# Kernel optimization log

Measured on AMD Instinct MI355X. Metric: run time of the kernel, lower is better.

## Reference

```python
import jax, jax.numpy as jnp
import numpy as np

L, H, D, FF = 6, 16, 768, 3072
B, N = 4, 1023
HD = D // H  # 48
EPS = 1e-5


def _layernorm(x, w, b):
    m = jnp.mean(x, axis=-1, keepdims=True)
    v = jnp.mean((x - m) ** 2, axis=-1, keepdims=True)
    return (x - m) / jnp.sqrt(v + EPS) * w + b


def setup_inputs() -> dict:
    key = jax.random.key(0)
    ks = jax.random.split(key, 10)
    ratio = 2.0 ** (-8.0 / H)
    slopes = np.array([ratio ** (i + 1) for i in range(H)], dtype=np.float32)
    return {
        "cls_tokens": jax.random.normal(ks[0], (B, N, D), jnp.float32),
        "cls_token": jax.random.normal(ks[1], (1, 1, D), jnp.float32) * 0.02,
        "log_slopes": jnp.log(jnp.asarray(slopes)),
        "Wqkv": jax.random.normal(ks[2], (L, 3 * D, D), jnp.float32) * 0.02,
        "Wo": jax.random.normal(ks[3], (L, D, D), jnp.float32) * 0.02,
        "Wg": jax.random.normal(ks[4], (L, FF, D), jnp.float32) * 0.02,
        "Wu": jax.random.normal(ks[5], (L, FF, D), jnp.float32) * 0.02,
        "Wd": jax.random.normal(ks[6], (L, D, FF), jnp.float32) * 0.02,
        "ln1_w": jnp.ones((L, D), jnp.float32),
        "ln1_b": jnp.zeros((L, D), jnp.float32),
        "ln2_w": jnp.ones((L, D), jnp.float32),
        "ln2_b": jnp.zeros((L, D), jnp.float32),
        "fin_w": jnp.ones((D,), jnp.float32),
        "fin_b": jnp.zeros((D,), jnp.float32),
    }


def reference(cls_tokens, cls_token, log_slopes, Wqkv, Wo, Wg, Wu, Wd,
              ln1_w, ln1_b, ln2_w, ln2_b, fin_w, fin_b):
    b, n, dmodel = cls_tokens.shape
    S = n + 1
    # learnable ALiBi: -exp(log_slope) * |i - j|, shape (H, S, S)
    pos = jnp.arange(S)
    dist = jnp.abs(pos[None, :] - pos[:, None]).astype(cls_tokens.dtype)
    bias = -(jnp.exp(log_slopes)[:, None, None] * dist[None, :, :])

    x = jnp.concatenate([jnp.broadcast_to(cls_token, (b, 1, dmodel)), cls_tokens], axis=1)
    scale = 1.0 / jnp.sqrt(jnp.asarray(HD, x.dtype))

    for l in range(L):
        h = _layernorm(x, ln1_w[l], ln1_b[l])
        qkv = jnp.einsum('bsd,ed->bse', h, Wqkv[l]).reshape(b, S, 3, H, HD)
        qkv = qkv.transpose(2, 0, 3, 1, 4)  # (3, B, H, S, hd)
        q, k, v = qkv[0], qkv[1], qkv[2]
        scores = jnp.einsum('bhqd,bhkd->bhqk', q, k) * scale + bias[None]
        attn = jax.nn.softmax(scores, axis=-1)
        o = jnp.einsum('bhqk,bhkd->bhqd', attn, v)
        o = o.transpose(0, 2, 1, 3).reshape(b, S, dmodel)
        x = x + jnp.einsum('bsd,ed->bse', o, Wo[l])
        h = _layernorm(x, ln2_w[l], ln2_b[l])
        gate = jax.nn.silu(jnp.einsum('bsd,fd->bsf', h, Wg[l]))
        up = jnp.einsum('bsd,fd->bsf', h, Wu[l])
        x = x + jnp.einsum('bsf,df->bsd', gate * up, Wd[l])

    return _layernorm(x[:, 0, :], fin_w, fin_b)
```

## Files before the change

kernel.cpp:

```cpp
#include <hip/hip_runtime.h>
#include <hip/hip_bf16.h>

#define LNUM 6
#define HNUM 16
#define DMODEL 768
#define FFDIM 3072
#define BATCH 4
#define NTOK 1023
#define SEQ 1024
#define HD 48
#define EPS 1e-5f

typedef __hip_bfloat16 bf16;

__device__ __forceinline__ unsigned short f2bf_raw(float f) {
  bf16 h = __float2bfloat16(f);
  union { bf16 h; unsigned short s; } u; u.h = h; return u.s;
}

template <int CTRL>
__device__ __forceinline__ float dppf(float x) {
  return __int_as_float(__builtin_amdgcn_update_dpp(
      0, __float_as_int(x), CTRL, 0xf, 0xf, true));
}
__device__ __forceinline__ float row_max16(float x) {
  x = fmaxf(x, dppf<0xB1>(x));
  x = fmaxf(x, dppf<0x4E>(x));
  x = fmaxf(x, dppf<0x124>(x));
  x = fmaxf(x, dppf<0x128>(x));
  return x;
}
__device__ __forceinline__ float row_sum16(float x) {
  x += dppf<0xB1>(x);
  x += dppf<0x4E>(x);
  x += dppf<0x124>(x);
  x += dppf<0x128>(x);
  return x;
}

__device__ __forceinline__ void xcd_swz(int& bx, int& by) {
  const int gx = gridDim.x;
  const int lin = blockIdx.y * gx + blockIdx.x;
  const int cpx = (gx * gridDim.y) >> 3;
  const int w = (lin & 7) * cpx + (lin >> 3);
  bx = w % gx;
  by = w / gx;
}

__global__ __launch_bounds__(256) void concat_kernel(
    const float* __restrict__ cls_tokens, const float* __restrict__ cls_token,
    float* __restrict__ x) {
  size_t i = (size_t)blockIdx.x * blockDim.x + threadIdx.x;
  const size_t total = (size_t)BATCH * SEQ * DMODEL;
  if (i >= total) return;
  int d = (int)(i % DMODEL);
  size_t bs = i / DMODEL;
  int s = (int)(bs % SEQ);
  int b = (int)(bs / SEQ);
  float v;
  if (s == 0) v = cls_token[d];
  else v = cls_tokens[((size_t)b * NTOK + (s - 1)) * DMODEL + d];
  x[i] = v;
}

#define W_QKV4  442368
#define W_O4    147456
#define W_FF4   589824
__global__ __launch_bounds__(256) void convert_w_kernel(
    const float* __restrict__ wqkv, const float* __restrict__ wo,
    const float* __restrict__ wg, const float* __restrict__ wu,
    const float* __restrict__ wd, bf16* __restrict__ dst) {
  size_t i4 = (size_t)blockIdx.x * 256 + threadIdx.x;
  size_t off4 = i4;
  const float* src;
  if (off4 < W_QKV4) src = wqkv;
  else { off4 -= W_QKV4;
    if (off4 < W_O4) src = wo;
    else { off4 -= W_O4;
      if (off4 < W_FF4) src = wg;
      else { off4 -= W_FF4;
        if (off4 < W_FF4) src = wu;
        else { off4 -= W_FF4; src = wd; } } } }
  float4 v = ((const float4*)src)[off4];
  ushort4 o;
  o.x = f2bf_raw(v.x); o.y = f2bf_raw(v.y);
  o.z = f2bf_raw(v.z); o.w = f2bf_raw(v.w);
  ((ushort4*)dst)[i4] = o;
}

__device__ __forceinline__ void st_ln(float* p, float v) { *p = v; }
__device__ __forceinline__ void st_ln(bf16* p, float v) { *p = __float2bfloat16(v); }

template <typename OUT>
__global__ __launch_bounds__(256) void ln_kernel(
    const float* __restrict__ in, OUT* __restrict__ out,
    const float* __restrict__ w, const float* __restrict__ bias,
    size_t in_stride, size_t out_stride) {
  const int row = blockIdx.x;
  const int tid = threadIdx.x;
  const float* x = in + (size_t)row * in_stride;
  OUT* y = out + (size_t)row * out_stride;

  float v0 = x[tid], v1 = x[tid + 256], v2 = x[tid + 512];
  float s = v0 + v1 + v2;
  float sq = v0 * v0 + v1 * v1 + v2 * v2;

  __shared__ float s_sum[256];
  __shared__ float s_sq[256];
  s_sum[tid] = s;
  s_sq[tid] = sq;
  __syncthreads();
  for (int off = 128; off > 0; off >>= 1) {
    if (tid < off) {
      s_sum[tid] += s_sum[tid + off];
      s_sq[tid] += s_sq[tid + off];
    }
    __syncthreads();
  }
  const float inv_d = 1.0f / (float)DMODEL;
  float mean = s_sum[0] * inv_d;
  float var = s_sq[0] * inv_d - mean * mean;
  float rstd = rsqrtf(var + EPS);

  st_ln(y + tid,       (v0 - mean) * rstd * w[tid]       + bias[tid]);
  st_ln(y + tid + 256, (v1 - mean) * rstd * w[tid + 256] + bias[tid + 256]);
  st_ln(y + tid + 512, (v2 - mean) * rstd * w[tid + 512] + bias[tid + 512]);
}

#define BM 128
#define BN 128
#define BK 32

typedef __attribute__((ext_vector_type(8))) short bfrag;
typedef __attribute__((ext_vector_type(4))) float f32x4;

__device__ __forceinline__ void async_copy16(const void* g, void* l) {
  __builtin_amdgcn_global_load_lds(
      (const __attribute__((address_space(1))) void*)g,
      (__attribute__((address_space(3))) void*)l, 16, 0, 0);
}

template <int CMODE>
__global__ __launch_bounds__(256) void gemm_bf16(
    const bf16* __restrict__ A, const bf16* __restrict__ B,
    void* __restrict__ Cv, int M, int N, int K) {
  __shared__ bf16 As[2][BM][BK];
  __shared__ bf16 Bs[2][BN][BK];

  const int tid = threadIdx.x;
  const int wave = tid >> 6;
  const int lane = tid & 63;
  int bx, by;
  xcd_swz(bx, by);
  const int m0 = by * BM;
  const int n0 = bx * BN;
  const int wm = (wave & 1) * 64;
  const int wn = (wave >> 1) * 64;

  f32x4 acc[4][4];
#pragma unroll
  for (int i = 0; i < 4; i++)
#pragma unroll
    for (int j = 0; j < 4; j++) acc[i][j] = (f32x4)(0.f);

  const int lrow = lane >> 2;
  const int lcol = (lane & 3) * 8;
  const bf16* Ag[2]; const bf16* Bg[2];
  void *AsB[2][2], *BsB[2][2];
#pragma unroll
  for (int j = 0; j < 2; j++) {
    int c = j * 4 + wave;
    Ag[j] = A + (size_t)(m0 + c * 16 + lrow) * K + lcol;
    Bg[j] = B + (size_t)(n0 + c * 16 + lrow) * K + lcol;
#pragma unroll
    for (int bf = 0; bf < 2; bf++) {
      AsB[bf][j] = (void*)&As[bf][c * 16][0];
      BsB[bf][j] = (void*)&Bs[bf][c * 16][0];
    }
  }

#pragma unroll
  for (int j = 0; j < 2; j++) {
    async_copy16(Ag[j], AsB[0][j]);
    async_copy16(Bg[j], BsB[0][j]);
  }

  const int fr = lane & 15;
  const int fk = (lane >> 4) * 8;
  const int nk = K / BK;

  for (int ki = 0; ki < nk; ki++) {
    const int cur = ki & 1;
    __syncthreads();
    if (ki + 1 < nk) {
      const int k0 = (ki + 1) * BK;
#pragma unroll
      for (int j = 0; j < 2; j++) {
        async_copy16(Ag[j] + k0, AsB[cur ^ 1][j]);
        async_copy16(Bg[j] + k0, BsB[cur ^ 1][j]);
      }
    }
    bfrag a[4], b[4];
#pragma unroll
    for (int i = 0; i < 4; i++) {
      a[i] = *(const bfrag*)&As[cur][wm + i * 16 + fr][fk];
      b[i] = *(const bfrag*)&Bs[cur][wn + i * 16 + fr][fk];
    }
#pragma unroll
    for (int i = 0; i < 4; i++)
#pragma unroll
      for (int j = 0; j < 4; j++)
        acc[i][j] = __builtin_amdgcn_mfma_f32_16x16x32_bf16(a[i], b[j], acc[i][j], 0, 0, 0);
  }

  const int ccol = lane & 15;
  const int crow = (lane >> 4) * 4;
#pragma unroll
  for (int i = 0; i < 4; i++) {
#pragma unroll
    for (int j = 0; j < 4; j++) {
#pragma unroll
      for (int r = 0; r < 4; r++) {
        const size_t gm = m0 + wm + i * 16 + crow + r;
        const size_t gn = n0 + wn + j * 16 + ccol;
        if (CMODE == 2) {
          ((bf16*)Cv)[gm * N + gn] = __float2bfloat16(acc[i][j][r]);
        } else if (CMODE == 1) {
          float* cp = (float*)Cv + gm * N + gn;
          *cp += acc[i][j][r];
        } else {
          ((float*)Cv)[gm * N + gn] = acc[i][j][r];
        }
      }
    }
  }
}

template <int CMODE, int SPLITK>
__global__ __launch_bounds__(256) void gemm_bf16_n64(
    const bf16* __restrict__ A, const bf16* __restrict__ B,
    void* __restrict__ Cv, int M, int N, int K) {
  __shared__ bf16 As[2][64][BK];
  __shared__ bf16 Bs[2][64][BK];

  const int tid = threadIdx.x;
  const int wave = tid >> 6;
  const int lane = tid & 63;
  int bx, by;
  xcd_swz(bx, by);
  const int m0 = by * 64;
  const int n0 = bx * 64;
  const int wm = (wave & 1) * 32;
  const int wn = (wave >> 1) * 32;
  const int koff = (SPLITK > 1) ? (int)blockIdx.z * (K / SPLITK) : 0;

  f32x4 acc[2][2];
#pragma unroll
  for (int i = 0; i < 2; i++)
#pragma unroll
    for (int j = 0; j < 2; j++) acc[i][j] = (f32x4)(0.f);

  const int srow = tid >> 2;
  const int scol = (tid & 3) * 8;
  const bf16* Ag = A + (size_t)(m0 + srow) * K + koff + scol;
  const bf16* Bg = B + (size_t)(n0 + srow) * K + koff + scol;
  void *AsB[2], *BsB[2];
#pragma unroll
  for (int bf = 0; bf < 2; bf++) {
    AsB[bf] = (void*)&As[bf][srow][scol];
    BsB[bf] = (void*)&Bs[bf][srow][scol];
  }

  async_copy16(Ag, AsB[0]);
  async_copy16(Bg, BsB[0]);

  const int fr = lane & 15;
  const int fk = (lane >> 4) * 8;
  const int nk = (K / SPLITK) / BK;

  for (int ki = 0; ki < nk; ki++) {
    const int cur = ki & 1;
    __syncthreads();
    if (ki + 1 < nk) {
      const int k0 = (ki + 1) * BK;
      async_copy16(Ag + k0, AsB[cur ^ 1]);
      async_copy16(Bg + k0, BsB[cur ^ 1]);
    }
    bfrag a[2], b[2];
#pragma unroll
    for (int i = 0; i < 2; i++)
      a[i] = *(const bfrag*)&As[cur][wm + i * 16 + fr][fk];
#pragma unroll
    for (int j = 0; j < 2; j++)
      b[j] = *(const bfrag*)&Bs[cur][wn + j * 16 + fr][fk];
#pragma unroll
    for (int i = 0; i < 2; i++)
#pragma unroll
      for (int j = 0; j < 2; j++)
        acc[i][j] = __builtin_amdgcn_mfma_f32_16x16x32_bf16(a[i], b[j], acc[i][j], 0, 0, 0);
  }

  const int ccol = lane & 15;
  const int crow = (lane >> 4) * 4;
#pragma unroll
  for (int i = 0; i < 2; i++) {
#pragma unroll
    for (int j = 0; j < 2; j++) {
#pragma unroll
      for (int r = 0; r < 4; r++) {
        const size_t gm = m0 + wm + i * 16 + crow + r;
        const size_t gn = n0 + wn + j * 16 + ccol;
        if (CMODE == 2) {
          ((bf16*)Cv)[gm * N + gn] = __float2bfloat16(acc[i][j][r]);
        } else if (CMODE == 1) {
          float* cp = (float*)Cv + gm * N + gn;
          if (SPLITK > 1) atomicAdd(cp, acc[i][j][r]);
          else *cp += acc[i][j][r];
        } else {
          ((float*)Cv)[gm * N + gn] = acc[i][j][r];
        }
      }
    }
  }
}

__global__ __launch_bounds__(256) void gemm_gateup(
    const bf16* __restrict__ A, const bf16* __restrict__ Wg,
    const bf16* __restrict__ Wu, bf16* __restrict__ gu, int M, int N, int K) {
  __shared__ bf16 As[2][BM][BK];
  __shared__ bf16 Gs[2][BN][BK];
  __shared__ bf16 Us[2][BN][BK];

  const int tid = threadIdx.x;
  const int wave = tid >> 6;
  const int lane = tid & 63;
  int bx, by;
  xcd_swz(bx, by);
  const int m0 = by * BM;
  const int n0 = bx * BN;
  const int wm = (wave & 1) * 64;
  const int wn = (wave >> 1) * 64;

  f32x4 accG[4][4], accU[4][4];
#pragma unroll
  for (int i = 0; i < 4; i++)
#pragma unroll
    for (int j = 0; j < 4; j++) { accG[i][j] = (f32x4)(0.f); accU[i][j] = (f32x4)(0.f); }

  const int lrow = lane >> 2;
  const int lcol = (lane & 3) * 8;
  const bf16 *Ag[2], *Gg[2], *Ug[2];
  void *AsB[2][2], *GsB[2][2], *UsB[2][2];
#pragma unroll
  for (int j = 0; j < 2; j++) {
    int c = j * 4 + wave;
    Ag[j] = A + (size_t)(m0 + c * 16 + lrow) * K + lcol;
    Gg[j] = Wg + (size_t)(n0 + c * 16 + lrow) * K + lcol;
    Ug[j] = Wu + (size_t)(n0 + c * 16 + lrow) * K + lcol;
#pragma unroll
    for (int bf = 0; bf < 2; bf++) {
      AsB[bf][j] = (void*)&As[bf][c * 16][0];
      GsB[bf][j] = (void*)&Gs[bf][c * 16][0];
      UsB[bf][j] = (void*)&Us[bf][c * 16][0];
    }
  }

#pragma unroll
  for (int j = 0; j < 2; j++) {
    async_copy16(Ag[j], AsB[0][j]);
    async_copy16(Gg[j], GsB[0][j]);
    async_copy16(Ug[j], UsB[0][j]);
  }

  const int fr = lane & 15;
  const int fk = (lane >> 4) * 8;
  const int nk = K / BK;

  for (int ki = 0; ki < nk; ki++) {
    const int cur = ki & 1;
    __syncthreads();
    if (ki + 1 < nk) {
      const int k0 = (ki + 1) * BK;
#pragma unroll
      for (int j = 0; j < 2; j++) {
        async_copy16(Ag[j] + k0, AsB[cur ^ 1][j]);
        async_copy16(Gg[j] + k0, GsB[cur ^ 1][j]);
        async_copy16(Ug[j] + k0, UsB[cur ^ 1][j]);
      }
    }
    bfrag a[4], g[4], u[4];
#pragma unroll
    for (int i = 0; i < 4; i++) {
      a[i] = *(const bfrag*)&As[cur][wm + i * 16 + fr][fk];
      g[i] = *(const bfrag*)&Gs[cur][wn + i * 16 + fr][fk];
      u[i] = *(const bfrag*)&Us[cur][wn + i * 16 + fr][fk];
    }
#pragma unroll
    for (int i = 0; i < 4; i++)
#pragma unroll
      for (int j = 0; j < 4; j++) {
        accG[i][j] = __builtin_amdgcn_mfma_f32_16x16x32_bf16(a[i], g[j], accG[i][j], 0, 0, 0);
        accU[i][j] = __builtin_amdgcn_mfma_f32_16x16x32_bf16(a[i], u[j], accU[i][j], 0, 0, 0);
      }
  }

  const int ccol = lane & 15;
  const int crow = (lane >> 4) * 4;
#pragma unroll
  for (int i = 0; i < 4; i++) {
#pragma unroll
    for (int j = 0; j < 4; j++) {
#pragma unroll
      for (int r = 0; r < 4; r++) {
        const size_t gm = m0 + wm + i * 16 + crow + r;
        const size_t gn = n0 + wn + j * 16 + ccol;
        const float gv = accG[i][j][r];
        const float uv = accU[i][j][r];
        const float res = gv / (1.0f + __expf(-gv)) * uv;
        gu[gm * N + gn] = __float2bfloat16(res);
      }
    }
  }
}

__global__ __launch_bounds__(256) void transpose_v(
    const bf16* __restrict__ qkv, bf16* __restrict__ vt) {
  __shared__ bf16 T[HD][64];
  const int tid = threadIdx.x;
  const int kb = blockIdx.x * 64;
  const int h = blockIdx.y;
  const int b = blockIdx.z;
  const size_t rstride = 3 * DMODEL;
  const bf16* vsrc = qkv + ((size_t)(b * SEQ + kb)) * rstride + 2 * DMODEL + h * HD;

  if (tid < 192) {
    int p = tid & 31, c = tid >> 5;
    const bf16* v0 = vsrc + (size_t)(2 * p) * rstride + c * 8;
    uint4 r0 = *(const uint4*)v0;
    uint4 r1 = *(const uint4*)(v0 + rstride);
    const unsigned int* w0 = (const unsigned int*)&r0;
    const unsigned int* w1 = (const unsigned int*)&r1;
#pragma unroll
    for (int i = 0; i < 8; i++) {
      unsigned int lo = (i & 1) ? (w0[i >> 1] >> 16) : (w0[i >> 1] & 0xffffu);
      unsigned int hi = (i & 1) ? (w1[i >> 1] >> 16) : (w1[i >> 1] & 0xffffu);
      *(unsigned int*)&T[c * 8 + i][2 * p] = lo | (hi << 16);
    }
  }
  __syncthreads();
  for (int it = tid; it < HD * 8; it += 256) {
    int d = it >> 3, c = it & 7;
    *(uint4*)(vt + ((size_t)((b * HNUM + h) * HD + d)) * SEQ + kb + c * 8) =
        *(const uint4*)&T[d][c * 8];
  }
}

#define AQT 64
#define AKT 128
#define ASTR 72
#define VSTR 136

__global__ __launch_bounds__(256, 4) void attn_mfma(
    const bf16* __restrict__ qkv, const bf16* __restrict__ vt,
    const float* __restrict__ log_slopes, bf16* __restrict__ obuf) {
  __shared__ bf16 QPs[AQT][ASTR];
  __shared__ bf16 Ks[AKT][ASTR];
  __shared__ bf16 Vs[HD][VSTR];

  const int tid = threadIdx.x;
  const int wq = tid >> 6;
  const int lane = tid & 63;
  const int l15 = lane & 15;
  const int lh = lane >> 4;

  const int id = blockIdx.x;
  const int w = (id & 7) * 128 + (id >> 3);
  const int qb = (w & 15) * AQT;
  const int h = (w >> 4) & 15;
  const int b = w >> 8;

  const float c1 = 0.14433756729740643f * 1.4426950408889634f;
  const float slope2 = __expf(log_slopes[h]) * 1.4426950408889634f;
  const size_t rstride = 3 * DMODEL;
  const bf16* qbase = qkv + ((size_t)(b * SEQ + qb)) * rstride + h * HD;
  const bf16* kbase0 = qkv + ((size_t)b * SEQ) * rstride + DMODEL + h * HD;
  const bf16* vbase0 = vt + ((size_t)((b * HNUM + h) * HD)) * SEQ;

  bf16* ldst[6];
  int goff[6];
#pragma unroll
  for (int j = 0; j < 6; j++) {
    if (j < 3) {
      int id2 = tid + j * 256;
      int r = id2 / 6, c = id2 - r * 6;
      ldst[j] = &Ks[r][c * 8];
      goff[j] = r * (int)rstride + c * 8;
    } else {
      int id3 = tid + (j - 3) * 256;
      int d = id3 >> 4, c = id3 & 15;
      ldst[j] = &Vs[d][c * 8];
      goff[j] = d * SEQ + c * 8;
    }
  }

  {
    int r = tid >> 1, c = tid & 1;
    *(uint4*)&Ks[r][48 + c * 8] = make_uint4(0, 0, 0, 0);
  }
  if (tid < 128) {
    int r = tid >> 1, c = tid & 1;
    *(uint4*)&QPs[r][48 + c * 8] = make_uint4(0, 0, 0, 0);
  }
  for (int it = tid; it < AQT * 6; it += 256) {
    int r = it / 6, c = it - (it / 6) * 6;
    *(uint4*)&QPs[r][c * 8] = *(const uint4*)(qbase + (size_t)r * rstride + c * 8);
  }
  __syncthreads();
  const bfrag aq0 = *(const bfrag*)&QPs[wq * 16 + l15][lh * 8];
  const bfrag aq1 = *(const bfrag*)&QPs[wq * 16 + l15][32 + lh * 8];

  uint4 pre[6];
#pragma unroll
  for (int j = 0; j < 6; j++)
    pre[j] = *(const uint4*)((j < 3 ? kbase0 : vbase0) + goff[j]);

  float m_[4], l_[4];
  f32x4 accO[3];
#pragma unroll
  for (int r = 0; r < 4; r++) { m_[r] = -1e30f; l_[r] = 0.f; }
#pragma unroll
  for (int t = 0; t < 3; t++) accO[t] = (f32x4)(0.f);

  for (int kb = 0; kb < SEQ; kb += AKT) {
    __syncthreads();
#pragma unroll
    for (int j = 0; j < 6; j++) *(uint4*)ldst[j] = pre[j];
    __syncthreads();
    if (kb + AKT < SEQ) {
      const bf16* kb1 = kbase0 + (size_t)(kb + AKT) * rstride;
      const bf16* vb1 = vbase0 + (kb + AKT);
#pragma unroll
      for (int j = 0; j < 6; j++)
        pre[j] = *(const uint4*)((j < 3 ? kb1 : vb1) + goff[j]);
    }

    f32x4 accS[8];
#pragma unroll
    for (int j = 0; j < 8; j++) accS[j] = (f32x4)(0.f);
    __builtin_amdgcn_s_setprio(1);
#pragma unroll
    for (int j = 0; j < 8; j++) {
      bfrag bk = *(const bfrag*)&Ks[j * 16 + l15][lh * 8];
      accS[j] = __builtin_amdgcn_mfma_f32_16x16x32_bf16(aq0, bk, accS[j], 0, 0, 0);
    }
#pragma unroll
    for (int j = 0; j < 8; j++) {
      bfrag bk = *(const bfrag*)&Ks[j * 16 + l15][32 + lh * 8];
      accS[j] = __builtin_amdgcn_mfma_f32_16x16x32_bf16(aq1, bk, accS[j], 0, 0, 0);
    }
    __builtin_amdgcn_s_setprio(0);

    float ps[8][4];
#pragma unroll
    for (int r = 0; r < 4; r++) {
      const float fq = (float)(qb + wq * 16 + lh * 4 + r);
      const float d0 = fq - (float)(kb + l15);
      float s[8];
#pragma unroll
      for (int j = 0; j < 8; j++)
        s[j] = fmaf(accS[j][r], c1, -slope2 * fabsf(d0 - 16.0f * (float)j));
      float mx = fmaxf(fmaxf(fmaxf(s[0], s[1]), fmaxf(s[2], s[3])),
                       fmaxf(fmaxf(s[4], s[5]), fmaxf(s[6], s[7])));
      mx = row_max16(mx);
      const float mnew = fmaxf(m_[r], mx);
      const float corr = exp2f(m_[r] - mnew);
      float rs = 0.f;
#pragma unroll
      for (int j = 0; j < 8; j++) {
        ps[j][r] = exp2f(s[j] - mnew);
        rs += ps[j][r];
      }
      rs = row_sum16(rs);
      l_[r] = l_[r] * corr + rs;
      m_[r] = mnew;
#pragma unroll
      for (int t = 0; t < 3; t++) accO[t][r] *= corr;
    }

#pragma unroll
    for (int half = 0; half < 2; half++) {
#pragma unroll
      for (int j2 = 0; j2 < 4; j2++)
#pragma unroll
        for (int r = 0; r < 4; r++)
          QPs[wq * 16 + lh * 4 + r][j2 * 16 + l15] =
              __float2bfloat16(ps[half * 4 + j2][r]);
#pragma unroll
      for (int ks = 0; ks < 2; ks++) {
        bfrag pa = *(const bfrag*)&QPs[wq * 16 + l15][ks * 32 + lh * 8];
        __builtin_amdgcn_s_setprio(1);
#pragma unroll
        for (int t = 0; t < 3; t++) {
          bfrag vb = *(const bfrag*)&Vs[t * 16 + l15][half * 64 + ks * 32 + lh * 8];
          accO[t] = __builtin_amdgcn_mfma_f32_16x16x32_bf16(pa, vb, accO[t], 0, 0, 0);
        }
        __builtin_amdgcn_s_setprio(0);
      }
    }
  }

#pragma unroll
  for (int r = 0; r < 4; r++) {
    const float inv = 1.0f / l_[r];
    bf16* op = obuf + ((size_t)(b * SEQ + qb + wq * 16 + lh * 4 + r)) * DMODEL + h * HD;
#pragma unroll
    for (int t = 0; t < 3; t++)
      op[t * 16 + l15] = __float2bfloat16(accO[t][r] * inv);
  }
}

extern "C" void kernel_launch(void* const* d_in, const int* in_sizes, int n_in,
                              void* d_out, int out_size, void* d_ws, size_t ws_size,
                              hipStream_t stream) {
  const float* cls_tokens = (const float*)d_in[0];
  const float* cls_token  = (const float*)d_in[1];
  const float* log_slopes = (const float*)d_in[2];
  const float* Wqkv = (const float*)d_in[3];
  const float* Wo   = (const float*)d_in[4];
  const float* Wg   = (const float*)d_in[5];
  const float* Wu   = (const float*)d_in[6];
  const float* Wd   = (const float*)d_in[7];
  const float* ln1_w = (const float*)d_in[8];
  const float* ln1_b = (const float*)d_in[9];
  const float* ln2_w = (const float*)d_in[10];
  const float* ln2_b = (const float*)d_in[11];
  const float* fin_w = (const float*)d_in[12];
  const float* fin_b = (const float*)d_in[13];
  float* out = (float*)d_out;

  const size_t ROWS = (size_t)BATCH * SEQ;
  char* wsb = (char*)d_ws;
  float* x    = (float*)(wsb);
  bf16* qkvb  = (bf16*)(wsb + 12582912);
  bf16* hb    = (bf16*)(wsb + 31457280);
  bf16* ob    = (bf16*)(wsb + 37748736);
  bf16* gub   = (bf16*)(wsb + 44040192);
  bf16* wbf   = (bf16*)(wsb + 94371840);
  bf16* vtb   = (bf16*)(wsb + 113246208);

  bf16* wqkv_b = wbf;
  bf16* wo_b   = wbf + 1769472;
  bf16* wg_b   = wbf + 2359296;
  bf16* wu_b   = wbf + 4718592;
  bf16* wd_b   = wbf + 7077888;

  {
    const size_t total = ROWS * DMODEL;
    concat_kernel<<<(int)((total + 255) / 256), 256, 0, stream>>>(cls_tokens, cls_token, x);
  }

  for (int l = 0; l < LNUM; l++) {
    convert_w_kernel<<<9216, 256, 0, stream>>>(
        Wqkv + (size_t)l * 3 * DMODEL * DMODEL, Wo + (size_t)l * DMODEL * DMODEL,
        Wg + (size_t)l * FFDIM * DMODEL, Wu + (size_t)l * FFDIM * DMODEL,
        Wd + (size_t)l * DMODEL * FFDIM, wbf);

    ln_kernel<bf16><<<(int)ROWS, 256, 0, stream>>>(
        x, hb, ln1_w + l * DMODEL, ln1_b + l * DMODEL, DMODEL, DMODEL);
    gemm_bf16<2><<<dim3(3 * DMODEL / BN, ROWS / BM), 256, 0, stream>>>(
        hb, wqkv_b, qkvb, (int)ROWS, 3 * DMODEL, DMODEL);
    transpose_v<<<dim3(SEQ / 64, HNUM, BATCH), 256, 0, stream>>>(qkvb, vtb);
    attn_mfma<<<dim3(SEQ / AQT * HNUM * BATCH), 256, 0, stream>>>(
        qkvb, vtb, log_slopes, ob);
    gemm_bf16_n64<1, 1><<<dim3(DMODEL / 64, ROWS / 64), 256, 0, stream>>>(
        ob, wo_b, x, (int)ROWS, DMODEL, DMODEL);
    ln_kernel<bf16><<<(int)ROWS, 256, 0, stream>>>(
        x, hb, ln2_w + l * DMODEL, ln2_b + l * DMODEL, DMODEL, DMODEL);
    gemm_gateup<<<dim3(FFDIM / BN, ROWS / BM), 256, 0, stream>>>(
        hb, wg_b, wu_b, gub, (int)ROWS, FFDIM, DMODEL);
    gemm_bf16_n64<1, 2><<<dim3(DMODEL / 64, ROWS / 64, 2), 256, 0, stream>>>(
        gub, wd_b, x, (int)ROWS, DMODEL, FFDIM);
  }

  ln_kernel<float><<<BATCH, 256, 0, stream>>>(x, out, fin_w, fin_b,
                                              (size_t)SEQ * DMODEL, DMODEL);
}
```

Measured before the change: 1.790 ms.

## Halve attention key tile and add lazy softmax rescaling

Shrinks the attention key/value tile from 128 to 64 keys, so K and V share a three-slot prefetch with smaller LDS buffers and fewer live registers. Adds a thresholded online-softmax update that skips max correction and accumulator rescaling unless the row max grows by more than 8 (log2 units) anywhere in the wave. This trades twice as many loop iterations and barriers for lower register/LDS pressure, better occupancy and fewer exp/rescale operations. The lazy rescale keeps the result exact in principle, but probabilities can reach up to 2^8 before bf16 conversion.

```diff
diff --git a/kernel.cpp b/kernel.cpp
--- a/kernel.cpp
+++ b/kernel.cpp
@@ -456,16 +456,15 @@
 }
 
 #define AQT 64
-#define AKT 128
+#define AKT 64
 #define ASTR 72
-#define VSTR 136
 
 __global__ __launch_bounds__(256, 4) void attn_mfma(
     const bf16* __restrict__ qkv, const bf16* __restrict__ vt,
     const float* __restrict__ log_slopes, bf16* __restrict__ obuf) {
   __shared__ bf16 QPs[AQT][ASTR];
   __shared__ bf16 Ks[AKT][ASTR];
-  __shared__ bf16 Vs[HD][VSTR];
+  __shared__ bf16 Vs[HD][ASTR];
 
   const int tid = threadIdx.x;
   const int wq = tid >> 6;
@@ -486,30 +485,30 @@
   const bf16* kbase0 = qkv + ((size_t)b * SEQ) * rstride + DMODEL + h * HD;
   const bf16* vbase0 = vt + ((size_t)((b * HNUM + h) * HD)) * SEQ;
 
-  bf16* ldst[6];
-  int goff[6];
-#pragma unroll
-  for (int j = 0; j < 6; j++) {
-    if (j < 3) {
-      int id2 = tid + j * 256;
+  bf16* ldst[3];
+  int goff[3];
+  bool isK[3];
+#pragma unroll
+  for (int j = 0; j < 3; j++) {
+    int id2 = tid + j * 256;
+    if (id2 < 384) {
       int r = id2 / 6, c = id2 - r * 6;
       ldst[j] = &Ks[r][c * 8];
       goff[j] = r * (int)rstride + c * 8;
+      isK[j] = true;
     } else {
-      int id3 = tid + (j - 3) * 256;
-      int d = id3 >> 4, c = id3 & 15;
+      id2 -= 384;
+      int d = id2 >> 3, c = id2 & 7;
       ldst[j] = &Vs[d][c * 8];
       goff[j] = d * SEQ + c * 8;
-    }
-  }
-
-  {
-    int r = tid >> 1, c = tid & 1;
+      isK[j] = false;
+    }
+  }
+
+  for (int it = tid; it < AQT * 2; it += 256) {
+    int r = it >> 1, c = it & 1;
+    *(uint4*)&QPs[r][48 + c * 8] = make_uint4(0, 0, 0, 0);
     *(uint4*)&Ks[r][48 + c * 8] = make_uint4(0, 0, 0, 0);
-  }
-  if (tid < 128) {
-    int r = tid >> 1, c = tid & 1;
-    *(uint4*)&QPs[r][48 + c * 8] = make_uint4(0, 0, 0, 0);
   }
   for (int it = tid; it < AQT * 6; it += 256) {
     int r = it / 6, c = it - (it / 6) * 6;
@@ -519,10 +518,10 @@
   const bfrag aq0 = *(const bfrag*)&QPs[wq * 16 + l15][lh * 8];
   const bfrag aq1 = *(const bfrag*)&QPs[wq * 16 + l15][32 + lh * 8];
 
-  uint4 pre[6];
-#pragma unroll
-  for (int j = 0; j < 6; j++)
-    pre[j] = *(const uint4*)((j < 3 ? kbase0 : vbase0) + goff[j]);
+  uint4 pre[3];
+#pragma unroll
+  for (int j = 0; j < 3; j++)
+    pre[j] = *(const uint4*)((isK[j] ? kbase0 : vbase0) + goff[j]);
 
   float m_[4], l_[4];
   f32x4 accO[3];
@@ -534,78 +533,77 @@
   for (int kb = 0; kb < SEQ; kb += AKT) {
     __syncthreads();
 #pragma unroll
-    for (int j = 0; j < 6; j++) *(uint4*)ldst[j] = pre[j];
+    for (int j = 0; j < 3; j++) *(uint4*)ldst[j] = pre[j];
     __syncthreads();
     if (kb + AKT < SEQ) {
       const bf16* kb1 = kbase0 + (size_t)(kb + AKT) * rstride;
       const bf16* vb1 = vbase0 + (kb + AKT);
 #pragma unroll
-      for (int j = 0; j < 6; j++)
-        pre[j] = *(const uint4*)((j < 3 ? kb1 : vb1) + goff[j]);
-    }
-
-    f32x4 accS[8];
-#pragma unroll
-    for (int j = 0; j < 8; j++) accS[j] = (f32x4)(0.f);
+      for (int j = 0; j < 3; j++)
+        pre[j] = *(const uint4*)((isK[j] ? kb1 : vb1) + goff[j]);
+    }
+
+    f32x4 accS[4];
+#pragma unroll
+    for (int j = 0; j < 4; j++) accS[j] = (f32x4)(0.f);
     __builtin_amdgcn_s_setprio(1);
 #pragma unroll
-    for (int j = 0; j < 8; j++) {
+    for (int j = 0; j < 4; j++) {
       bfrag bk = *(const bfrag*)&Ks[j * 16 + l15][lh * 8];
       accS[j] = __builtin_amdgcn_mfma_f32_16x16x32_bf16(aq0, bk, accS[j], 0, 0, 0);
     }
 #pragma unroll
-    for (int j = 0; j < 8; j++) {
+    for (int j = 0; j < 4; j++) {
       bfrag bk = *(const bfrag*)&Ks[j * 16 + l15][32 + lh * 8];
       accS[j] = __builtin_amdgcn_mfma_f32_16x16x32_bf16(aq1, bk, accS[j], 0, 0, 0);
     }
     __builtin_amdgcn_s_setprio(0);
 
-    float ps[8][4];
+    float ps[4][4];
 #pragma unroll
     for (int r = 0; r < 4; r++) {
       const float fq = (float)(qb + wq * 16 + lh * 4 + r);
-      const float d0 = fq - (float)(kb + l15);
-      float s[8];
-#pragma unroll
-      for (int j = 0; j < 8; j++)
-        s[j] = fmaf(accS[j][r], c1, -slope2 * fabsf(d0 - 16.0f * (float)j));
-      float mx = fmaxf(fmaxf(fmaxf(s[0], s[1]), fmaxf(s[2], s[3])),
-                       fmaxf(fmaxf(s[4], s[5]), fmaxf(s[6], s[7])));
-      mx = row_max16(mx);
-      const float mnew = fmaxf(m_[r], mx);
-      const float corr = exp2f(m_[r] - mnew);
+      float s[4];
+#pragma unroll
+      for (int j = 0; j < 4; j++) {
+        const float fk = (float)(kb + j * 16 + l15);
+        s[j] = fmaf(accS[j][r], c1, -slope2 * fabsf(fq - fk));
+      }
+      float mx = row_max16(fmaxf(fmaxf(s[0], s[1]), fmaxf(s[2], s[3])));
+      if (!__all(mx - m_[r] <= 8.0f)) {
+        const float mnew = fmaxf(m_[r], mx);
+        const float corr = exp2f(m_[r] - mnew);
+        l_[r] *= corr;
+#pragma unroll
+        for (int t = 0; t < 3; t++) accO[t][r] *= corr;
+        m_[r] = mnew;
+      }
       float rs = 0.f;
 #pragma unroll
-      for (int j = 0; j < 8; j++) {
-        ps[j][r] = exp2f(s[j] - mnew);
+      for (int j = 0; j < 4; j++) {
+        ps[j][r] = exp2f(s[j] - m_[r]);
         rs += ps[j][r];
       }
       rs = row_sum16(rs);
-      l_[r] = l_[r] * corr + rs;
-      m_[r] = mnew;
-#pragma unroll
-      for (int t = 0; t < 3; t++) accO[t][r] *= corr;
-    }
-
-#pragma unroll
-    for (int half = 0; half < 2; half++) {
-#pragma unroll
-      for (int j2 = 0; j2 < 4; j2++)
-#pragma unroll
-        for (int r = 0; r < 4; r++)
-          QPs[wq * 16 + lh * 4 + r][j2 * 16 + l15] =
-              __float2bfloat16(ps[half * 4 + j2][r]);
-#pragma unroll
-      for (int ks = 0; ks < 2; ks++) {
-        bfrag pa = *(const bfrag*)&QPs[wq * 16 + l15][ks * 32 + lh * 8];
-        __builtin_amdgcn_s_setprio(1);
-#pragma unroll
-        for (int t = 0; t < 3; t++) {
-          bfrag vb = *(const bfrag*)&Vs[t * 16 + l15][half * 64 + ks * 32 + lh * 8];
-          accO[t] = __builtin_amdgcn_mfma_f32_16x16x32_bf16(pa, vb, accO[t], 0, 0, 0);
-        }
-        __builtin_amdgcn_s_setprio(0);
-      }
+      l_[r] += rs;
+    }
+
+#pragma unroll
+    for (int j = 0; j < 4; j++)
+#pragma unroll
+      for (int r = 0; r < 4; r++)
+        QPs[wq * 16 + lh * 4 + r][j * 16 + l15] = __float2bfloat16(ps[j][r]);
+
+#pragma unroll
+    for (int ks = 0; ks < 2; ks++) {
+      bfrag pa = *(const bfrag*)&QPs[wq * 16 + l15][ks * 32 + lh * 8];
+      __builtin_amdgcn_s_setprio(1);
+#pragma unroll
+      for (int t = 0; t < 3; t++) {
+        bfrag vb = *(const bfrag*)&Vs[t * 16 + l15][ks * 32 + lh * 8];
+        accO[t] = __builtin_amdgcn_mfma_f32_16x16x32_bf16(pa, vb, accO[t], 0, 0, 0);
+      }
+      __builtin_amdgcn_s_setprio(0);
     }
   }
 
```

New measurement: 1.765 ms. About the same (-1.4%).
